# Performance work log

Measured on AMD Instinct MI355X. Metric: run time of the kernel, lower is better.

Reference implementation:

```python
import jax, jax.numpy as jnp
import numpy as np

B = 4096      # batch
F = 26        # num sparse features
L = 10        # pooling factor (multi-hot indices per feature)
V = 100000    # rows per embedding table
D = 128       # embedding dim (== dense_arch_layer_sizes[-1])
DENSE_IN = 13
DENSE_SIZES = [512, 256, 128]
OVER_SIZES = [1024, 1024, 512, 256, 1]
OVER_IN = D + (F * (F - 1)) // 2 + F  # 479


def _linear_params(key, dims, prefix):
    out = {}
    ks = jax.random.split(key, len(dims) - 1)
    for i in range(len(dims) - 1):
        fan_in = dims[i]
        out[f"{prefix}W{i}"] = jax.random.normal(ks[i], (dims[i], dims[i + 1]), jnp.float32) / np.sqrt(fan_in)
        out[f"{prefix}b{i}"] = jnp.zeros((dims[i + 1],), jnp.float32)
    return out


def setup_inputs() -> dict:
    key = jax.random.key(0)
    k0, k1, k2, k3, k4 = jax.random.split(key, 5)
    inp = {
        "dense_features": jax.random.normal(k0, (B, DENSE_IN), jnp.float32),
        "indices": jax.random.randint(k1, (B, F, L), 0, V, dtype=jnp.int64),
        "tables": jax.random.normal(k2, (F, V, D), jnp.float32) * 0.01,
    }
    inp.update(_linear_params(k3, [DENSE_IN] + DENSE_SIZES, "d"))
    inp.update(_linear_params(k4, [OVER_IN] + OVER_SIZES, "o"))
    return inp


def _dlrm_forward(dense_features, indices, tables,
                  dW0, db0, dW1, db1, dW2, db2,
                  oW0, ob0, oW1, ob1, oW2, ob2, oW3, ob3, oW4, ob4):
    b = dense_features.shape[0]
    # DenseArch: MLP with relu on every layer
    x = dense_features
    for W, bb in ((dW0, db0), (dW1, db1), (dW2, db2)):
        x = jax.nn.relu(x @ W + bb)
    embedded_dense = x  # [B, D]

    # SparseArch: pooled (sum) embedding lookup per feature -> [B, F, D]
    flat_tables = tables.reshape(F * V, D)
    offs = jnp.arange(F, dtype=indices.dtype) * V
    flat_idx = (indices + offs[None, :, None]).reshape(-1)
    gathered = jnp.take(flat_tables, flat_idx, axis=0).reshape(b, F, L, D)
    embedded_sparse = gathered.sum(axis=2)  # [B, F, D]

    # InteractionArch: bmm + upper-triangular gather
    z = jnp.concatenate([embedded_dense[:, None, :], embedded_sparse], axis=1)  # [B, F+1, D]
    inter = jnp.einsum("bnd,bmd->bnm", z, z)  # [B, F+1, F+1]
    iu0, iu1 = np.triu_indices(F + 1, k=1)
    inter_flat = inter[:, iu0, iu1]  # [B, C(F+1,2)]
    feats = jnp.concatenate([embedded_dense, inter_flat], axis=1)  # [B, OVER_IN]

    # OverArch: relu MLP on layer_sizes[:-1], then plain final Linear
    y = feats
    for W, bb in ((oW0, ob0), (oW1, ob1), (oW2, ob2), (oW3, ob3)):
        y = jax.nn.relu(y @ W + bb)
    logits = y @ oW4 + ob4  # [B, 1]
    return logits


def reference(dense_features, indices, tables,
              dW0, db0, dW1, db1, dW2, db2,
              oW0, ob0, oW1, ob1, oW2, ob2, oW3, ob3, oW4, ob4):
    return _dlrm_forward(dense_features, indices, tables,
                         dW0, db0, dW1, db1, dW2, db2,
                         oW0, ob0, oW1, ob1, oW2, ob2, oW3, ob3, oW4, ob4)
```

## Files before the change

kernel.cpp:

```cpp
#include <hip/hip_runtime.h>

#define B_ 4096
#define F_ 26
#define L_ 10
#define V_ 100000
#define D_ 128

typedef __attribute__((ext_vector_type(8))) short short8;
typedef __attribute__((ext_vector_type(4))) float f32x4;

__device__ inline unsigned pack_split(float f) {
    union { float f; unsigned u; } a; a.f = f;
    unsigned r = (a.u + 0x7FFFu + ((a.u >> 16) & 1u)) >> 16;
    union { unsigned u; float f; } hf; hf.u = r << 16;
    float rem = f - hf.f;
    union { float f; unsigned u; } b; b.f = rem;
    unsigned r2 = (b.u + 0x7FFFu + ((b.u >> 16) & 1u)) >> 16;
    return (r << 16) | (r2 & 0xFFFFu);
}
__device__ inline float unpack_f(unsigned u) {
    union { unsigned u; float f; } h; h.u = u & 0xFFFF0000u;
    union { unsigned u; float f; } l; l.u = u << 16;
    return h.f + l.f;
}

__device__ void prep_tile(const float* __restrict__ W, unsigned* __restrict__ Wt,
                          int K, int N, int Kp, int local)
{
    __shared__ float tile[32][33];
    const int t = threadIdx.x;
    const int tx = t & 31, ty = t >> 5;
    const int nbt = N >> 5;
    const int nb = (local % nbt) << 5, kb = (local / nbt) << 5;
    #pragma unroll
    for (int i = 0; i < 4; ++i) {
        int k = kb + ty + i * 8;
        tile[ty + i * 8][tx] = (k < K) ? W[(size_t)k * N + nb + tx] : 0.f;
    }
    __syncthreads();
    #pragma unroll
    for (int i = 0; i < 4; ++i) {
        int nl = ty + i * 8;
        Wt[(size_t)(nb + nl) * Kp + kb + tx] = pack_split(tile[tx][nl]);
    }
}

__global__ __launch_bounds__(256) void prep_all(
    const float* dW0, const float* dW1, const float* dW2,
    const float* oW0, const float* oW1, const float* oW2, const float* oW3,
    unsigned* dWt0, unsigned* dWt1, unsigned* dWt2,
    unsigned* oWt0, unsigned* oWt1, unsigned* oWt2, unsigned* oWt3,
    const float* dense, unsigned* densep)
{
    const int bid = blockIdx.x;
    if      (bid < 16)   prep_tile(dW0, dWt0, 13,   512,  32,   bid);
    else if (bid < 144)  prep_tile(dW1, dWt1, 512,  256,  512,  bid - 16);
    else if (bid < 176)  prep_tile(dW2, dWt2, 256,  128,  256,  bid - 144);
    else if (bid < 656)  prep_tile(oW0, oWt0, 479,  1024, 480,  bid - 176);
    else if (bid < 1680) prep_tile(oW1, oWt1, 1024, 1024, 1024, bid - 656);
    else if (bid < 2192) prep_tile(oW2, oWt2, 1024, 512,  1024, bid - 1680);
    else if (bid < 2320) prep_tile(oW3, oWt3, 512,  256,  512,  bid - 2192);
    else {
        int g = (bid - 2320) * 256 + threadIdx.x;
        int b = g >> 5, k = g & 31;
        densep[g] = (k < 13) ? pack_split(dense[(size_t)b * 13 + k]) : 0u;
    }
}

template<bool RELU>
__global__ __launch_bounds__(512) void gemm8(
    const unsigned* __restrict__ Ap, const unsigned* __restrict__ Wt,
    const float* __restrict__ bias, unsigned* __restrict__ Cp,
    int M, int N, int Kp)
{
    __shared__ __align__(16) unsigned Au[2][128 * 32];
    __shared__ __align__(16) unsigned Bu[2][128 * 32];

    const int t    = threadIdx.x;
    const int lane = t & 63;
    const int w    = t >> 6;
    const int wm   = w >> 2, wn = w & 3;
    const int m0   = blockIdx.y * 128, n0 = blockIdx.x * 128;

    f32x4 acc[4][2];
    const f32x4 zero = {0.f, 0.f, 0.f, 0.f};
    #pragma unroll
    for (int i = 0; i < 4; ++i)
        #pragma unroll
        for (int j = 0; j < 2; ++j) acc[i][j] = zero;

    const unsigned* Ab = Ap + (size_t)m0 * Kp;
    const unsigned* Bb = Wt + (size_t)n0 * Kp;

    const int g4 = lane >> 4;
    const int rr = lane & 15;

    auto STAGE = [&](int buf, int k0) {
        #pragma unroll
        for (int i = 0; i < 2; ++i) {
            int chunk = t + (i << 9);
            int row = chunk >> 3, ch = chunk & 7;
            int sch = ch ^ (row & 7);
            __builtin_amdgcn_global_load_lds(
                (const __attribute__((address_space(1))) unsigned*)(Ab + (size_t)row * Kp + k0 + (sch << 2)),
                &Au[buf][chunk << 2], 16, 0, 0);
        }
        #pragma unroll
        for (int i = 0; i < 2; ++i) {
            int chunk = t + (i << 9);
            int row = chunk >> 3, ch = chunk & 7;
            int sch = ch ^ (row & 7);
            __builtin_amdgcn_global_load_lds(
                (const __attribute__((address_space(1))) unsigned*)(Bb + (size_t)row * Kp + k0 + (sch << 2)),
                &Bu[buf][chunk << 2], 16, 0, 0);
        }
    };

    auto COMPUTE = [&](int buf) {
        const unsigned* au = Au[buf];
        const unsigned* bu = Bu[buf];
        short8 bh[2], bl[2];
        #pragma unroll
        for (int tj = 0; tj < 2; ++tj) {
            int r = wn * 32 + tj * 16 + rr;
            int c0 = (2 * g4) ^ (r & 7), c1 = (2 * g4 + 1) ^ (r & 7);
            uint4 p = *reinterpret_cast<const uint4*>(&bu[r * 32 + (c0 << 2)]);
            uint4 q = *reinterpret_cast<const uint4*>(&bu[r * 32 + (c1 << 2)]);
            union { short8 s; uint4 u; } H, L;
            H.u.x = __builtin_amdgcn_perm(p.y, p.x, 0x07060302u);
            L.u.x = __builtin_amdgcn_perm(p.y, p.x, 0x05040100u);
            H.u.y = __builtin_amdgcn_perm(p.w, p.z, 0x07060302u);
            L.u.y = __builtin_amdgcn_perm(p.w, p.z, 0x05040100u);
            H.u.z = __builtin_amdgcn_perm(q.y, q.x, 0x07060302u);
            L.u.z = __builtin_amdgcn_perm(q.y, q.x, 0x05040100u);
            H.u.w = __builtin_amdgcn_perm(q.w, q.z, 0x07060302u);
            L.u.w = __builtin_amdgcn_perm(q.w, q.z, 0x05040100u);
            bh[tj] = H.s; bl[tj] = L.s;
        }
        #pragma unroll
        for (int ti = 0; ti < 4; ++ti) {
            int r = wm * 64 + ti * 16 + rr;
            int c0 = (2 * g4) ^ (r & 7), c1 = (2 * g4 + 1) ^ (r & 7);
            uint4 p = *reinterpret_cast<const uint4*>(&au[r * 32 + (c0 << 2)]);
            uint4 q = *reinterpret_cast<const uint4*>(&au[r * 32 + (c1 << 2)]);
            union { short8 s; uint4 u; } H, L;
            H.u.x = __builtin_amdgcn_perm(p.y, p.x, 0x07060302u);
            L.u.x = __builtin_amdgcn_perm(p.y, p.x, 0x05040100u);
            H.u.y = __builtin_amdgcn_perm(p.w, p.z, 0x07060302u);
            L.u.y = __builtin_amdgcn_perm(p.w, p.z, 0x05040100u);
            H.u.z = __builtin_amdgcn_perm(q.y, q.x, 0x07060302u);
            L.u.z = __builtin_amdgcn_perm(q.y, q.x, 0x05040100u);
            H.u.w = __builtin_amdgcn_perm(q.w, q.z, 0x07060302u);
            L.u.w = __builtin_amdgcn_perm(q.w, q.z, 0x05040100u);
            short8 ah = H.s, al = L.s;
            #pragma unroll
            for (int tj = 0; tj < 2; ++tj) {
                f32x4 c = acc[ti][tj];
                c = __builtin_amdgcn_mfma_f32_16x16x32_bf16(ah, bh[tj], c, 0, 0, 0);
                c = __builtin_amdgcn_mfma_f32_16x16x32_bf16(ah, bl[tj], c, 0, 0, 0);
                c = __builtin_amdgcn_mfma_f32_16x16x32_bf16(al, bh[tj], c, 0, 0, 0);
                acc[ti][tj] = c;
            }
        }
    };

    const int nt = Kp >> 5;
    STAGE(0, 0);
    __syncthreads();
    int cur = 0;
    for (int ts = 0; ts < nt - 1; ++ts) {
        STAGE(cur ^ 1, (ts + 1) << 5);
        COMPUTE(cur);
        __syncthreads();
        cur ^= 1;
    }
    COMPUTE(cur);

    #pragma unroll
    for (int ti = 0; ti < 4; ++ti) {
        int row = m0 + wm * 64 + ti * 16 + (g4 << 2);
        #pragma unroll
        for (int tj = 0; tj < 2; ++tj) {
            int col = n0 + wn * 32 + tj * 16 + rr;
            float bv = bias[col];
            #pragma unroll
            for (int r = 0; r < 4; ++r) {
                float v = acc[ti][tj][r] + bv;
                if (RELU) v = fmaxf(v, 0.f);
                Cp[(size_t)(row + r) * N + col] = pack_split(v);
            }
        }
    }
}

__global__ __launch_bounds__(256) void gather_interact_mfma(
    const unsigned* __restrict__ x2p,
    const int*      __restrict__ idx_words,
    const float*    __restrict__ tables,
    unsigned*       __restrict__ featsp)
{
    __shared__ unsigned zh[4][32][64];
    __shared__ unsigned zl[4][32][64];
    __shared__ int sidx[4][F_ * L_];
    __shared__ int sstride;

    const int t    = threadIdx.x;
    const int w    = t >> 6;
    const int lane = t & 63;
    const int s    = blockIdx.x * 4 + w;

    if (t == 0) {
        int st = 2;
        for (int ww = 1; ww < 256; ww += 2)
            if (idx_words[ww] != 0) { st = 1; break; }
        sstride = st;
    }
    __syncthreads();
    const int st = sstride;

    for (int q = lane; q < F_ * L_; q += 64) {
        int v = idx_words[((size_t)s * F_ * L_ + q) * st];
        sidx[w][q] = v < 0 ? 0 : (v >= V_ ? V_ - 1 : v);
    }
    uint2 xv = *reinterpret_cast<const uint2*>(x2p + (size_t)s * 128 + 2 * lane);
    *reinterpret_cast<uint2*>(featsp + (size_t)s * 480 + 2 * lane) = xv;
    if (lane == 0) featsp[(size_t)s * 480 + 479] = 0u;
    zh[w][0][lane] = (xv.x >> 16) | (xv.y & 0xFFFF0000u);
    zl[w][0][lane] = (xv.x & 0xFFFFu) | (xv.y << 16);
    __syncthreads();

    for (int f = 0; f < F_; ++f) {
        float2 a = {0.f, 0.f};
        const float* tab = tables + (size_t)f * V_ * D_;
        #pragma unroll
        for (int l = 0; l < L_; ++l) {
            int idx = sidx[w][f * L_ + l];
            float2 v = *reinterpret_cast<const float2*>(tab + (size_t)idx * D_ + 2 * lane);
            a.x += v.x; a.y += v.y;
        }
        unsigned px = pack_split(a.x), py = pack_split(a.y);
        int r  = f + 1;
        int dw = (((lane >> 2) ^ (r & 7)) << 2) + (lane & 3);
        zh[w][r][dw] = (px >> 16) | (py & 0xFFFF0000u);
        zl[w][r][dw] = (px & 0xFFFFu) | (py << 16);
    }
    __syncthreads();

    const int g4 = lane >> 4;
    const int rr = lane & 15;
    f32x4 acc[2][2];
    const f32x4 zero = {0.f, 0.f, 0.f, 0.f};
    acc[0][0] = zero; acc[0][1] = zero; acc[1][0] = zero; acc[1][1] = zero;

    #pragma unroll
    for (int ks = 0; ks < 4; ++ks) {
        short8 h[2], lo[2];
        #pragma unroll
        for (int mi = 0; mi < 2; ++mi) {
            int r = mi * 16 + rr;
            int c = (ks * 4 + g4) ^ (r & 7);
            h[mi]  = *reinterpret_cast<const short8*>(&zh[w][r][c << 2]);
            lo[mi] = *reinterpret_cast<const short8*>(&zl[w][r][c << 2]);
        }
        #pragma unroll
        for (int mi = 0; mi < 2; ++mi)
            #pragma unroll
            for (int nj = 0; nj < 2; ++nj) {
                f32x4 c = acc[mi][nj];
                c = __builtin_amdgcn_mfma_f32_16x16x32_bf16(h[mi],  h[nj],  c, 0, 0, 0);
                c = __builtin_amdgcn_mfma_f32_16x16x32_bf16(h[mi],  lo[nj], c, 0, 0, 0);
                c = __builtin_amdgcn_mfma_f32_16x16x32_bf16(lo[mi], h[nj],  c, 0, 0, 0);
                acc[mi][nj] = c;
            }
    }

    #pragma unroll
    for (int mi = 0; mi < 2; ++mi) {
        #pragma unroll
        for (int nj = 0; nj < 2; ++nj) {
            #pragma unroll
            for (int r = 0; r < 4; ++r) {
                int i = mi * 16 + g4 * 4 + r;
                int j = nj * 16 + rr;
                if (i < j && j <= 26) {
                    int p = i * 26 - (i * (i - 1)) / 2 + (j - i - 1);
                    featsp[(size_t)s * 480 + 128 + p] = pack_split(acc[mi][nj][r]);
                }
            }
        }
    }
}

__global__ __launch_bounds__(256) void final_dot(
    const unsigned* __restrict__ yp, const float* __restrict__ w,
    const float* __restrict__ bias, float* __restrict__ out)
{
    const int wave = threadIdx.x >> 6;
    const int lane = threadIdx.x & 63;
    const int b = blockIdx.x * 4 + wave;
    uint4 u = *reinterpret_cast<const uint4*>(yp + (size_t)b * 256 + lane * 4);
    float4 wv = *reinterpret_cast<const float4*>(&w[lane * 4]);
    float s = unpack_f(u.x) * wv.x + unpack_f(u.y) * wv.y +
              unpack_f(u.z) * wv.z + unpack_f(u.w) * wv.w;
    #pragma unroll
    for (int off = 32; off; off >>= 1) s += __shfl_xor(s, off);
    if (lane == 0) out[b] = s + bias[0];
}

extern "C" void kernel_launch(void* const* d_in, const int* in_sizes, int n_in,
                              void* d_out, int out_size, void* d_ws, size_t ws_size,
                              hipStream_t stream)
{
    const float* dense   = (const float*)d_in[0];
    const int*   indices = (const int*)  d_in[1];
    const float* tables  = (const float*)d_in[2];
    const float* dW0 = (const float*)d_in[3];  const float* db0 = (const float*)d_in[4];
    const float* dW1 = (const float*)d_in[5];  const float* db1 = (const float*)d_in[6];
    const float* dW2 = (const float*)d_in[7];  const float* db2 = (const float*)d_in[8];
    const float* oW0 = (const float*)d_in[9];  const float* ob0 = (const float*)d_in[10];
    const float* oW1 = (const float*)d_in[11]; const float* ob1 = (const float*)d_in[12];
    const float* oW2 = (const float*)d_in[13]; const float* ob2 = (const float*)d_in[14];
    const float* oW3 = (const float*)d_in[15]; const float* ob3 = (const float*)d_in[16];
    const float* oW4 = (const float*)d_in[17]; const float* ob4 = (const float*)d_in[18];
    float* out = (float*)d_out;

    unsigned* wsu = (unsigned*)d_ws;
    unsigned* dWt0 = wsu + 0;
    unsigned* dWt1 = wsu + 16384;
    unsigned* dWt2 = wsu + 147456;
    unsigned* oWt0 = wsu + 180224;
    unsigned* oWt1 = wsu + 671744;
    unsigned* oWt2 = wsu + 1720320;
    unsigned* oWt3 = wsu + 2244608;
    unsigned* densep = wsu + 2375680;
    unsigned* x2p    = wsu + 2506752;
    unsigned* featsp = wsu + 3031040;
    unsigned* x0p    = wsu + 5000000;
    unsigned* x1p    = wsu + 7097152;
    unsigned* y0p    = wsu + 5000000;
    unsigned* y1p    = wsu + 9194304;
    unsigned* y2p    = wsu + 2506752;
    unsigned* y3p    = wsu + 5000000;

    prep_all<<<2832, 256, 0, stream>>>(dW0, dW1, dW2, oW0, oW1, oW2, oW3,
                                       dWt0, dWt1, dWt2, oWt0, oWt1, oWt2, oWt3,
                                       dense, densep);

    gemm8<true><<<dim3(4, B_ / 128), 512, 0, stream>>>(densep, dWt0, db0, x0p, B_, 512, 32);
    gemm8<true><<<dim3(2, B_ / 128), 512, 0, stream>>>(x0p,    dWt1, db1, x1p, B_, 256, 512);
    gemm8<true><<<dim3(1, B_ / 128), 512, 0, stream>>>(x1p,    dWt2, db2, x2p, B_, 128, 256);

    gather_interact_mfma<<<B_ / 4, 256, 0, stream>>>(x2p, indices, tables, featsp);

    gemm8<true><<<dim3(8, B_ / 128), 512, 0, stream>>>(featsp, oWt0, ob0, y0p, B_, 1024, 480);
    gemm8<true><<<dim3(8, B_ / 128), 512, 0, stream>>>(y0p,    oWt1, ob1, y1p, B_, 1024, 1024);
    gemm8<true><<<dim3(4, B_ / 128), 512, 0, stream>>>(y1p,    oWt2, ob2, y2p, B_, 512, 1024);
    gemm8<true><<<dim3(2, B_ / 128), 512, 0, stream>>>(y2p,    oWt3, ob3, y3p, B_, 256, 512);

    final_dot<<<B_ / 4, 256, 0, stream>>>(y3p, oW4, ob4, out);
}
```

Baseline: 294.6 us.

## Add 64-row GEMM tile variant, XCD-aware block swizzle, and paired-feature gather

```diff
diff --git a/kernel.cpp b/kernel.cpp
--- a/kernel.cpp
+++ b/kernel.cpp
@@ -67,20 +67,27 @@
     }
 }
 
-template<bool RELU>
-__global__ __launch_bounds__(512) void gemm8(
+template<int TM>
+__device__ __forceinline__ void gemm_body(
     const unsigned* __restrict__ Ap, const unsigned* __restrict__ Wt,
     const float* __restrict__ bias, unsigned* __restrict__ Cp,
-    int M, int N, int Kp)
-{
-    __shared__ __align__(16) unsigned Au[2][128 * 32];
+    int N, int Kp, int gx)
+{
+    constexpr int BT = TM * 4;
+    __shared__ __align__(16) unsigned Au[2][TM * 32];
     __shared__ __align__(16) unsigned Bu[2][128 * 32];
 
     const int t    = threadIdx.x;
     const int lane = t & 63;
     const int w    = t >> 6;
-    const int wm   = w >> 2, wn = w & 3;
-    const int m0   = blockIdx.y * 128, n0 = blockIdx.x * 128;
+    const int wm   = (TM == 128) ? (w >> 2) : 0;
+    const int wn   = (TM == 128) ? (w & 3) : w;
+
+    const int bid  = blockIdx.x;
+    const int cpx  = gridDim.x >> 3;
+    const int swz  = (bid & 7) * cpx + (bid >> 3);
+    const int n0   = (swz % gx) * 128;
+    const int m0   = (swz / gx) * TM;
 
     f32x4 acc[4][2];
     const f32x4 zero = {0.f, 0.f, 0.f, 0.f};
@@ -98,7 +105,7 @@
     auto STAGE = [&](int buf, int k0) {
         #pragma unroll
         for (int i = 0; i < 2; ++i) {
-            int chunk = t + (i << 9);
+            int chunk = t + i * BT;
             int row = chunk >> 3, ch = chunk & 7;
             int sch = ch ^ (row & 7);
             __builtin_amdgcn_global_load_lds(
@@ -106,8 +113,8 @@
                 &Au[buf][chunk << 2], 16, 0, 0);
         }
         #pragma unroll
-        for (int i = 0; i < 2; ++i) {
-            int chunk = t + (i << 9);
+        for (int i = 0; i < 1024 / BT; ++i) {
+            int chunk = t + i * BT;
             int row = chunk >> 3, ch = chunk & 7;
             int sch = ch ^ (row & 7);
             __builtin_amdgcn_global_load_lds(
@@ -185,12 +192,27 @@
             float bv = bias[col];
             #pragma unroll
             for (int r = 0; r < 4; ++r) {
-                float v = acc[ti][tj][r] + bv;
-                if (RELU) v = fmaxf(v, 0.f);
+                float v = fmaxf(acc[ti][tj][r] + bv, 0.f);
                 Cp[(size_t)(row + r) * N + col] = pack_split(v);
             }
         }
     }
+}
+
+__global__ __launch_bounds__(512) void gemm_t128(
+    const unsigned* __restrict__ Ap, const unsigned* __restrict__ Wt,
+    const float* __restrict__ bias, unsigned* __restrict__ Cp,
+    int N, int Kp, int gx)
+{
+    gemm_body<128>(Ap, Wt, bias, Cp, N, Kp, gx);
+}
+
+__global__ __launch_bounds__(256) void gemm_t64(
+    const unsigned* __restrict__ Ap, const unsigned* __restrict__ Wt,
+    const float* __restrict__ bias, unsigned* __restrict__ Cp,
+    int N, int Kp, int gx)
+{
+    gemm_body<64>(Ap, Wt, bias, Cp, N, Kp, gx);
 }
 
 __global__ __launch_bounds__(256) void gather_interact_mfma(
@@ -229,20 +251,33 @@
     zl[w][0][lane] = (xv.x & 0xFFFFu) | (xv.y << 16);
     __syncthreads();
 
-    for (int f = 0; f < F_; ++f) {
-        float2 a = {0.f, 0.f};
-        const float* tab = tables + (size_t)f * V_ * D_;
+    for (int f = 0; f < F_; f += 2) {
+        float2 a0 = {0.f, 0.f}, a1 = {0.f, 0.f};
+        const float* tab0 = tables + (size_t)f * V_ * D_;
+        const float* tab1 = tables + (size_t)(f + 1) * V_ * D_;
         #pragma unroll
         for (int l = 0; l < L_; ++l) {
-            int idx = sidx[w][f * L_ + l];
-            float2 v = *reinterpret_cast<const float2*>(tab + (size_t)idx * D_ + 2 * lane);
-            a.x += v.x; a.y += v.y;
-        }
-        unsigned px = pack_split(a.x), py = pack_split(a.y);
-        int r  = f + 1;
-        int dw = (((lane >> 2) ^ (r & 7)) << 2) + (lane & 3);
-        zh[w][r][dw] = (px >> 16) | (py & 0xFFFF0000u);
-        zl[w][r][dw] = (px & 0xFFFFu) | (py << 16);
+            int i0 = sidx[w][f * L_ + l];
+            int i1 = sidx[w][(f + 1) * L_ + l];
+            float2 v0 = *reinterpret_cast<const float2*>(tab0 + (size_t)i0 * D_ + 2 * lane);
+            float2 v1 = *reinterpret_cast<const float2*>(tab1 + (size_t)i1 * D_ + 2 * lane);
+            a0.x += v0.x; a0.y += v0.y;
+            a1.x += v1.x; a1.y += v1.y;
+        }
+        {
+            unsigned px = pack_split(a0.x), py = pack_split(a0.y);
+            int r  = f + 1;
+            int dw = (((lane >> 2) ^ (r & 7)) << 2) + (lane & 3);
+            zh[w][r][dw] = (px >> 16) | (py & 0xFFFF0000u);
+            zl[w][r][dw] = (px & 0xFFFFu) | (py << 16);
+        }
+        {
+            unsigned px = pack_split(a1.x), py = pack_split(a1.y);
+            int r  = f + 2;
+            int dw = (((lane >> 2) ^ (r & 7)) << 2) + (lane & 3);
+            zh[w][r][dw] = (px >> 16) | (py & 0xFFFF0000u);
+            zl[w][r][dw] = (px & 0xFFFFu) | (py << 16);
+        }
     }
     __syncthreads();
 
@@ -346,16 +381,16 @@
                                        dWt0, dWt1, dWt2, oWt0, oWt1, oWt2, oWt3,
                                        dense, densep);
 
-    gemm8<true><<<dim3(4, B_ / 128), 512, 0, stream>>>(densep, dWt0, db0, x0p, B_, 512, 32);
-    gemm8<true><<<dim3(2, B_ / 128), 512, 0, stream>>>(x0p,    dWt1, db1, x1p, B_, 256, 512);
-    gemm8<true><<<dim3(1, B_ / 128), 512, 0, stream>>>(x1p,    dWt2, db2, x2p, B_, 128, 256);
+    gemm_t64<<<4 * 64, 256, 0, stream>>>(densep, dWt0, db0, x0p, 512, 32,  4);
+    gemm_t64<<<2 * 64, 256, 0, stream>>>(x0p,    dWt1, db1, x1p, 256, 512, 2);
+    gemm_t64<<<1 * 64, 256, 0, stream>>>(x1p,    dWt2, db2, x2p, 128, 256, 1);
 
     gather_interact_mfma<<<B_ / 4, 256, 0, stream>>>(x2p, indices, tables, featsp);
 
-    gemm8<true><<<dim3(8, B_ / 128), 512, 0, stream>>>(featsp, oWt0, ob0, y0p, B_, 1024, 480);
-    gemm8<true><<<dim3(8, B_ / 128), 512, 0, stream>>>(y0p,    oWt1, ob1, y1p, B_, 1024, 1024);
-    gemm8<true><<<dim3(4, B_ / 128), 512, 0, stream>>>(y1p,    oWt2, ob2, y2p, B_, 512, 1024);
-    gemm8<true><<<dim3(2, B_ / 128), 512, 0, stream>>>(y2p,    oWt3, ob3, y3p, B_, 256, 512);
+    gemm_t128<<<8 * 32, 512, 0, stream>>>(featsp, oWt0, ob0, y0p, 1024, 480,  8);
+    gemm_t128<<<8 * 32, 512, 0, stream>>>(y0p,    oWt1, ob1, y1p, 1024, 1024, 8);
+    gemm_t64<<<4 * 64, 256, 0, stream>>>(y1p,    oWt2, ob2, y2p, 512, 1024, 4);
+    gemm_t64<<<2 * 64, 256, 0, stream>>>(y2p,    oWt3, ob3, y3p, 256, 512,  2);
 
     final_dot<<<B_ / 4, 256, 0, stream>>>(y3p, oW4, ob4, out);
 }
```

Result: no change. 299.3 us (+1.6%).

## Store split-bf16 operands as separate hi/lo planes to drop perm unpacking

Applied to the files above, without the earlier changes.

```diff
diff --git a/kernel.cpp b/kernel.cpp
--- a/kernel.cpp
+++ b/kernel.cpp
@@ -8,6 +8,7 @@
 
 typedef __attribute__((ext_vector_type(8))) short short8;
 typedef __attribute__((ext_vector_type(4))) float f32x4;
+typedef unsigned short u16;
 
 __device__ inline unsigned pack_split(float f) {
     union { float f; unsigned u; } a; a.f = f;
@@ -18,13 +19,13 @@
     unsigned r2 = (b.u + 0x7FFFu + ((b.u >> 16) & 1u)) >> 16;
     return (r << 16) | (r2 & 0xFFFFu);
 }
-__device__ inline float unpack_f(unsigned u) {
-    union { unsigned u; float f; } h; h.u = u & 0xFFFF0000u;
-    union { unsigned u; float f; } l; l.u = u << 16;
-    return h.f + l.f;
-}
-
-__device__ void prep_tile(const float* __restrict__ W, unsigned* __restrict__ Wt,
+__device__ inline float bf2_to_f(u16 h, u16 l) {
+    union { unsigned u; float f; } a; a.u = ((unsigned)h) << 16;
+    union { unsigned u; float f; } b; b.u = ((unsigned)l) << 16;
+    return a.f + b.f;
+}
+
+__device__ void prep_tile(const float* __restrict__ W, u16* __restrict__ Wt,
                           int K, int N, int Kp, int local)
 {
     __shared__ float tile[32][33];
@@ -41,16 +42,19 @@
     #pragma unroll
     for (int i = 0; i < 4; ++i) {
         int nl = ty + i * 8;
-        Wt[(size_t)(nb + nl) * Kp + kb + tx] = pack_split(tile[tx][nl]);
+        unsigned u = pack_split(tile[tx][nl]);
+        size_t base = (size_t)(nb + nl) * 2 * Kp + kb + tx;
+        Wt[base]      = (u16)(u >> 16);
+        Wt[base + Kp] = (u16)(u & 0xFFFFu);
     }
 }
 
 __global__ __launch_bounds__(256) void prep_all(
     const float* dW0, const float* dW1, const float* dW2,
     const float* oW0, const float* oW1, const float* oW2, const float* oW3,
-    unsigned* dWt0, unsigned* dWt1, unsigned* dWt2,
-    unsigned* oWt0, unsigned* oWt1, unsigned* oWt2, unsigned* oWt3,
-    const float* dense, unsigned* densep)
+    u16* dWt0, u16* dWt1, u16* dWt2,
+    u16* oWt0, u16* oWt1, u16* oWt2, u16* oWt3,
+    const float* dense, u16* densep)
 {
     const int bid = blockIdx.x;
     if      (bid < 16)   prep_tile(dW0, dWt0, 13,   512,  32,   bid);
@@ -63,18 +67,19 @@
     else {
         int g = (bid - 2320) * 256 + threadIdx.x;
         int b = g >> 5, k = g & 31;
-        densep[g] = (k < 13) ? pack_split(dense[(size_t)b * 13 + k]) : 0u;
-    }
-}
-
-template<bool RELU>
-__global__ __launch_bounds__(512) void gemm8(
-    const unsigned* __restrict__ Ap, const unsigned* __restrict__ Wt,
-    const float* __restrict__ bias, unsigned* __restrict__ Cp,
-    int M, int N, int Kp)
-{
-    __shared__ __align__(16) unsigned Au[2][128 * 32];
-    __shared__ __align__(16) unsigned Bu[2][128 * 32];
+        unsigned u = (k < 13) ? pack_split(dense[(size_t)b * 13 + k]) : 0u;
+        densep[(size_t)b * 64 + k]      = (u16)(u >> 16);
+        densep[(size_t)b * 64 + 32 + k] = (u16)(u & 0xFFFFu);
+    }
+}
+
+__global__ __launch_bounds__(512) void gemm_pl(
+    const u16* __restrict__ Ap, const u16* __restrict__ Wt,
+    const float* __restrict__ bias, u16* __restrict__ Cp,
+    int N, int Kp)
+{
+    __shared__ __align__(16) u16 Au[2][128 * 64];
+    __shared__ __align__(16) u16 Bu[2][128 * 64];
 
     const int t    = threadIdx.x;
     const int lane = t & 63;
@@ -89,8 +94,8 @@
         #pragma unroll
         for (int j = 0; j < 2; ++j) acc[i][j] = zero;
 
-    const unsigned* Ab = Ap + (size_t)m0 * Kp;
-    const unsigned* Bb = Wt + (size_t)n0 * Kp;
+    const u16* Ab = Ap + (size_t)m0 * 2 * Kp;
+    const u16* Bb = Wt + (size_t)n0 * 2 * Kp;
 
     const int g4 = lane >> 4;
     const int rr = lane & 15;
@@ -99,60 +104,44 @@
         #pragma unroll
         for (int i = 0; i < 2; ++i) {
             int chunk = t + (i << 9);
-            int row = chunk >> 3, ch = chunk & 7;
-            int sch = ch ^ (row & 7);
+            int row = chunk >> 3, c = chunk & 7;
+            int l = c ^ (row & 7);
             __builtin_amdgcn_global_load_lds(
-                (const __attribute__((address_space(1))) unsigned*)(Ab + (size_t)row * Kp + k0 + (sch << 2)),
-                &Au[buf][chunk << 2], 16, 0, 0);
+                (const __attribute__((address_space(1))) u16*)
+                    (Ab + (size_t)row * 2 * Kp + (l >> 2) * Kp + k0 + ((l & 3) << 3)),
+                &Au[buf][chunk << 3], 16, 0, 0);
         }
         #pragma unroll
         for (int i = 0; i < 2; ++i) {
             int chunk = t + (i << 9);
-            int row = chunk >> 3, ch = chunk & 7;
-            int sch = ch ^ (row & 7);
+            int row = chunk >> 3, c = chunk & 7;
+            int l = c ^ (row & 7);
             __builtin_amdgcn_global_load_lds(
-                (const __attribute__((address_space(1))) unsigned*)(Bb + (size_t)row * Kp + k0 + (sch << 2)),
-                &Bu[buf][chunk << 2], 16, 0, 0);
+                (const __attribute__((address_space(1))) u16*)
+                    (Bb + (size_t)row * 2 * Kp + (l >> 2) * Kp + k0 + ((l & 3) << 3)),
+                &Bu[buf][chunk << 3], 16, 0, 0);
         }
     };
 
     auto COMPUTE = [&](int buf) {
-        const unsigned* au = Au[buf];
-        const unsigned* bu = Bu[buf];
+        const u16* au = Au[buf];
+        const u16* bu = Bu[buf];
         short8 bh[2], bl[2];
         #pragma unroll
         for (int tj = 0; tj < 2; ++tj) {
             int r = wn * 32 + tj * 16 + rr;
-            int c0 = (2 * g4) ^ (r & 7), c1 = (2 * g4 + 1) ^ (r & 7);
-            uint4 p = *reinterpret_cast<const uint4*>(&bu[r * 32 + (c0 << 2)]);
-            uint4 q = *reinterpret_cast<const uint4*>(&bu[r * 32 + (c1 << 2)]);
-            union { short8 s; uint4 u; } H, L;
-            H.u.x = __builtin_amdgcn_perm(p.y, p.x, 0x07060302u);
-            L.u.x = __builtin_amdgcn_perm(p.y, p.x, 0x05040100u);
-            H.u.y = __builtin_amdgcn_perm(p.w, p.z, 0x07060302u);
-            L.u.y = __builtin_amdgcn_perm(p.w, p.z, 0x05040100u);
-            H.u.z = __builtin_amdgcn_perm(q.y, q.x, 0x07060302u);
-            L.u.z = __builtin_amdgcn_perm(q.y, q.x, 0x05040100u);
-            H.u.w = __builtin_amdgcn_perm(q.w, q.z, 0x07060302u);
-            L.u.w = __builtin_amdgcn_perm(q.w, q.z, 0x05040100u);
-            bh[tj] = H.s; bl[tj] = L.s;
+            int ch = (g4 ^ (r & 7)) << 3;
+            int cl = ((4 + g4) ^ (r & 7)) << 3;
+            bh[tj] = *reinterpret_cast<const short8*>(&bu[r * 64 + ch]);
+            bl[tj] = *reinterpret_cast<const short8*>(&bu[r * 64 + cl]);
         }
         #pragma unroll
         for (int ti = 0; ti < 4; ++ti) {
             int r = wm * 64 + ti * 16 + rr;
-            int c0 = (2 * g4) ^ (r & 7), c1 = (2 * g4 + 1) ^ (r & 7);
-            uint4 p = *reinterpret_cast<const uint4*>(&au[r * 32 + (c0 << 2)]);
-            uint4 q = *reinterpret_cast<const uint4*>(&au[r * 32 + (c1 << 2)]);
-            union { short8 s; uint4 u; } H, L;
-            H.u.x = __builtin_amdgcn_perm(p.y, p.x, 0x07060302u);
-            L.u.x = __builtin_amdgcn_perm(p.y, p.x, 0x05040100u);
-            H.u.y = __builtin_amdgcn_perm(p.w, p.z, 0x07060302u);
-            L.u.y = __builtin_amdgcn_perm(p.w, p.z, 0x05040100u);
-            H.u.z = __builtin_amdgcn_perm(q.y, q.x, 0x07060302u);
-            L.u.z = __builtin_amdgcn_perm(q.y, q.x, 0x05040100u);
-            H.u.w = __builtin_amdgcn_perm(q.w, q.z, 0x07060302u);
-            L.u.w = __builtin_amdgcn_perm(q.w, q.z, 0x05040100u);
-            short8 ah = H.s, al = L.s;
+            int ch = (g4 ^ (r & 7)) << 3;
+            int cl = ((4 + g4) ^ (r & 7)) << 3;
+            short8 ah = *reinterpret_cast<const short8*>(&au[r * 64 + ch]);
+            short8 al = *reinterpret_cast<const short8*>(&au[r * 64 + cl]);
             #pragma unroll
             for (int tj = 0; tj < 2; ++tj) {
                 f32x4 c = acc[ti][tj];
@@ -185,19 +174,21 @@
             float bv = bias[col];
             #pragma unroll
             for (int r = 0; r < 4; ++r) {
-                float v = acc[ti][tj][r] + bv;
-                if (RELU) v = fmaxf(v, 0.f);
-                Cp[(size_t)(row + r) * N + col] = pack_split(v);
+                float v = fmaxf(acc[ti][tj][r] + bv, 0.f);
+                unsigned u = pack_split(v);
+                size_t base = (size_t)(row + r) * 2 * N + col;
+                Cp[base]     = (u16)(u >> 16);
+                Cp[base + N] = (u16)(u & 0xFFFFu);
             }
         }
     }
 }
 
 __global__ __launch_bounds__(256) void gather_interact_mfma(
-    const unsigned* __restrict__ x2p,
-    const int*      __restrict__ idx_words,
-    const float*    __restrict__ tables,
-    unsigned*       __restrict__ featsp)
+    const u16*   __restrict__ x2p,
+    const int*   __restrict__ idx_words,
+    const float* __restrict__ tables,
+    u16*         __restrict__ featsp)
 {
     __shared__ unsigned zh[4][32][64];
     __shared__ unsigned zl[4][32][64];
@@ -222,11 +213,13 @@
         int v = idx_words[((size_t)s * F_ * L_ + q) * st];
         sidx[w][q] = v < 0 ? 0 : (v >= V_ ? V_ - 1 : v);
     }
-    uint2 xv = *reinterpret_cast<const uint2*>(x2p + (size_t)s * 128 + 2 * lane);
-    *reinterpret_cast<uint2*>(featsp + (size_t)s * 480 + 2 * lane) = xv;
-    if (lane == 0) featsp[(size_t)s * 480 + 479] = 0u;
-    zh[w][0][lane] = (xv.x >> 16) | (xv.y & 0xFFFF0000u);
-    zl[w][0][lane] = (xv.x & 0xFFFFu) | (xv.y << 16);
+    unsigned hv = *reinterpret_cast<const unsigned*>(x2p + (size_t)s * 256 + 2 * lane);
+    unsigned lv = *reinterpret_cast<const unsigned*>(x2p + (size_t)s * 256 + 128 + 2 * lane);
+    *reinterpret_cast<unsigned*>(featsp + (size_t)s * 960 + 2 * lane) = hv;
+    *reinterpret_cast<unsigned*>(featsp + (size_t)s * 960 + 480 + 2 * lane) = lv;
+    if (lane == 0) { featsp[(size_t)s * 960 + 479] = 0; featsp[(size_t)s * 960 + 959] = 0; }
+    zh[w][0][lane] = hv;
+    zl[w][0][lane] = lv;
     __syncthreads();
 
     for (int f = 0; f < F_; ++f) {
@@ -284,7 +277,9 @@
                 int j = nj * 16 + rr;
                 if (i < j && j <= 26) {
                     int p = i * 26 - (i * (i - 1)) / 2 + (j - i - 1);
-                    featsp[(size_t)s * 480 + 128 + p] = pack_split(acc[mi][nj][r]);
+                    unsigned u = pack_split(acc[mi][nj][r]);
+                    featsp[(size_t)s * 960 + 128 + p]       = (u16)(u >> 16);
+                    featsp[(size_t)s * 960 + 480 + 128 + p] = (u16)(u & 0xFFFFu);
                 }
             }
         }
@@ -292,16 +287,18 @@
 }
 
 __global__ __launch_bounds__(256) void final_dot(
-    const unsigned* __restrict__ yp, const float* __restrict__ w,
+    const u16* __restrict__ yp, const float* __restrict__ w,
     const float* __restrict__ bias, float* __restrict__ out)
 {
     const int wave = threadIdx.x >> 6;
     const int lane = threadIdx.x & 63;
     const int b = blockIdx.x * 4 + wave;
-    uint4 u = *reinterpret_cast<const uint4*>(yp + (size_t)b * 256 + lane * 4);
+    const u16* row = yp + (size_t)b * 512;
+    ushort4 uh = *reinterpret_cast<const ushort4*>(row + 4 * lane);
+    ushort4 ul = *reinterpret_cast<const ushort4*>(row + 256 + 4 * lane);
     float4 wv = *reinterpret_cast<const float4*>(&w[lane * 4]);
-    float s = unpack_f(u.x) * wv.x + unpack_f(u.y) * wv.y +
-              unpack_f(u.z) * wv.z + unpack_f(u.w) * wv.w;
+    float s = bf2_to_f(uh.x, ul.x) * wv.x + bf2_to_f(uh.y, ul.y) * wv.y +
+              bf2_to_f(uh.z, ul.z) * wv.z + bf2_to_f(uh.w, ul.w) * wv.w;
     #pragma unroll
     for (int off = 32; off; off >>= 1) s += __shfl_xor(s, off);
     if (lane == 0) out[b] = s + bias[0];
@@ -325,37 +322,37 @@
     float* out = (float*)d_out;
 
     unsigned* wsu = (unsigned*)d_ws;
-    unsigned* dWt0 = wsu + 0;
-    unsigned* dWt1 = wsu + 16384;
-    unsigned* dWt2 = wsu + 147456;
-    unsigned* oWt0 = wsu + 180224;
-    unsigned* oWt1 = wsu + 671744;
-    unsigned* oWt2 = wsu + 1720320;
-    unsigned* oWt3 = wsu + 2244608;
-    unsigned* densep = wsu + 2375680;
-    unsigned* x2p    = wsu + 2506752;
-    unsigned* featsp = wsu + 3031040;
-    unsigned* x0p    = wsu + 5000000;
-    unsigned* x1p    = wsu + 7097152;
-    unsigned* y0p    = wsu + 5000000;
-    unsigned* y1p    = wsu + 9194304;
-    unsigned* y2p    = wsu + 2506752;
-    unsigned* y3p    = wsu + 5000000;
+    u16* dWt0 = (u16*)(wsu + 0);
+    u16* dWt1 = (u16*)(wsu + 16384);
+    u16* dWt2 = (u16*)(wsu + 147456);
+    u16* oWt0 = (u16*)(wsu + 180224);
+    u16* oWt1 = (u16*)(wsu + 671744);
+    u16* oWt2 = (u16*)(wsu + 1720320);
+    u16* oWt3 = (u16*)(wsu + 2244608);
+    u16* densep = (u16*)(wsu + 2375680);
+    u16* x2p    = (u16*)(wsu + 2506752);
+    u16* featsp = (u16*)(wsu + 3031040);
+    u16* x0p    = (u16*)(wsu + 5000000);
+    u16* x1p    = (u16*)(wsu + 7097152);
+    u16* y0p    = (u16*)(wsu + 5000000);
+    u16* y1p    = (u16*)(wsu + 9194304);
+    u16* y2p    = (u16*)(wsu + 2506752);
+    u16* y3p    = (u16*)(wsu + 5000000);
 
     prep_all<<<2832, 256, 0, stream>>>(dW0, dW1, dW2, oW0, oW1, oW2, oW3,
                                        dWt0, dWt1, dWt2, oWt0, oWt1, oWt2, oWt3,
                                        dense, densep);
 
-    gemm8<true><<<dim3(4, B_ / 128), 512, 0, stream>>>(densep, dWt0, db0, x0p, B_, 512, 32);
-    gemm8<true><<<dim3(2, B_ / 128), 512, 0, stream>>>(x0p,    dWt1, db1, x1p, B_, 256, 512);
-    gemm8<true><<<dim3(1, B_ / 128), 512, 0, stream>>>(x1p,    dWt2, db2, x2p, B_, 128, 256);
+    gemm_pl<<<dim3(4, 32), 512, 0, stream>>>(densep, dWt0, db0, x0p, 512, 32);
+    gemm_pl<<<dim3(2, 32), 512, 0, stream>>>(x0p,    dWt1, db1, x1p, 256, 512);
+    gemm_pl<<<dim3(1, 32), 512, 0, stream>>>(x1p,    dWt2, db2, x2p, 128, 256);
 
     gather_interact_mfma<<<B_ / 4, 256, 0, stream>>>(x2p, indices, tables, featsp);
 
-    gemm8<true><<<dim3(8, B_ / 128), 512, 0, stream>>>(featsp, oWt0, ob0, y0p, B_, 1024, 480);
-    gemm8<true><<<dim3(8, B_ / 128), 512, 0, stream>>>(y0p,    oWt1, ob1, y1p, B_, 1024, 1024);
-    gemm8<true><<<dim3(4, B_ / 128), 512, 0, stream>>>(y1p,    oWt2, ob2, y2p, B_, 512, 1024);
-    gemm8<true><<<dim3(2, B_ / 128), 512, 0, stream>>>(y2p,    oWt3, ob3, y3p, B_, 256, 512);
+    gemm_pl<<<dim3(8, 32), 512, 0, stream>>>(featsp, oWt0, ob0, y0p, 1024, 480);
+    gemm_pl<<<dim3(8, 32), 512, 0, stream>>>(y0p,    oWt1, ob1, y1p, 1024, 1024);
+    gemm_pl<<<dim3(4, 32), 512, 0, stream>>>(y1p,    oWt2, ob2, y2p, 512, 1024);
+    gemm_pl<<<dim3(2, 32), 512, 0, stream>>>(y2p,    oWt3, ob3, y3p, 256, 512);
 
     final_dot<<<B_ / 4, 256, 0, stream>>>(y3p, oW4, ob4, out);
 }
```

New measurement: 302.6 us. 2.7% more time.

## Triple-buffer A tiles with vmcnt waits and one barrier per k-step in GEMM

Applied to the files above, without the earlier changes.

```diff
diff --git a/kernel.cpp b/kernel.cpp
--- a/kernel.cpp
+++ b/kernel.cpp
@@ -67,13 +67,12 @@
     }
 }
 
-template<bool RELU>
 __global__ __launch_bounds__(512) void gemm8(
     const unsigned* __restrict__ Ap, const unsigned* __restrict__ Wt,
     const float* __restrict__ bias, unsigned* __restrict__ Cp,
-    int M, int N, int Kp)
-{
-    __shared__ __align__(16) unsigned Au[2][128 * 32];
+    int N, int Kp)
+{
+    __shared__ __align__(16) unsigned Au[3][128 * 32];
     __shared__ __align__(16) unsigned Bu[2][128 * 32];
 
     const int t    = threadIdx.x;
@@ -95,7 +94,8 @@
     const int g4 = lane >> 4;
     const int rr = lane & 15;
 
-    auto STAGE = [&](int buf, int k0) {
+    auto STAGE_A = [&](int buf, int kt) {
+        int k0 = kt << 5;
         #pragma unroll
         for (int i = 0; i < 2; ++i) {
             int chunk = t + (i << 9);
@@ -105,6 +105,9 @@
                 (const __attribute__((address_space(1))) unsigned*)(Ab + (size_t)row * Kp + k0 + (sch << 2)),
                 &Au[buf][chunk << 2], 16, 0, 0);
         }
+    };
+    auto STAGE_B = [&](int buf, int kt) {
+        int k0 = kt << 5;
         #pragma unroll
         for (int i = 0; i < 2; ++i) {
             int chunk = t + (i << 9);
@@ -116,9 +119,9 @@
         }
     };
 
-    auto COMPUTE = [&](int buf) {
-        const unsigned* au = Au[buf];
-        const unsigned* bu = Bu[buf];
+    auto COMPUTE = [&](int abuf, int bbuf) {
+        const unsigned* au = Au[abuf];
+        const unsigned* bu = Bu[bbuf];
         short8 bh[2], bl[2];
         #pragma unroll
         for (int tj = 0; tj < 2; ++tj) {
@@ -165,16 +168,19 @@
     };
 
     const int nt = Kp >> 5;
-    STAGE(0, 0);
-    __syncthreads();
-    int cur = 0;
-    for (int ts = 0; ts < nt - 1; ++ts) {
-        STAGE(cur ^ 1, (ts + 1) << 5);
-        COMPUTE(cur);
-        __syncthreads();
-        cur ^= 1;
-    }
-    COMPUTE(cur);
+    STAGE_A(0, 0);
+    STAGE_B(0, 0);
+    if (nt > 1) STAGE_A(1, 1);
+
+    for (int ts = 0; ts < nt; ++ts) {
+        if (ts < nt - 1) asm volatile("s_waitcnt vmcnt(2)" ::: "memory");
+        else             asm volatile("s_waitcnt vmcnt(0)" ::: "memory");
+        __builtin_amdgcn_s_barrier();
+        __builtin_amdgcn_sched_barrier(0);
+        if (ts + 1 < nt) STAGE_B((ts + 1) & 1, ts + 1);
+        if (ts + 2 < nt) STAGE_A((ts + 2) % 3, ts + 2);
+        COMPUTE(ts % 3, ts & 1);
+    }
 
     #pragma unroll
     for (int ti = 0; ti < 4; ++ti) {
@@ -185,8 +191,7 @@
             float bv = bias[col];
             #pragma unroll
             for (int r = 0; r < 4; ++r) {
-                float v = acc[ti][tj][r] + bv;
-                if (RELU) v = fmaxf(v, 0.f);
+                float v = fmaxf(acc[ti][tj][r] + bv, 0.f);
                 Cp[(size_t)(row + r) * N + col] = pack_split(v);
             }
         }
@@ -346,16 +351,16 @@
                                        dWt0, dWt1, dWt2, oWt0, oWt1, oWt2, oWt3,
                                        dense, densep);
 
-    gemm8<true><<<dim3(4, B_ / 128), 512, 0, stream>>>(densep, dWt0, db0, x0p, B_, 512, 32);
-    gemm8<true><<<dim3(2, B_ / 128), 512, 0, stream>>>(x0p,    dWt1, db1, x1p, B_, 256, 512);
-    gemm8<true><<<dim3(1, B_ / 128), 512, 0, stream>>>(x1p,    dWt2, db2, x2p, B_, 128, 256);
+    gemm8<<<dim3(4, 32), 512, 0, stream>>>(densep, dWt0, db0, x0p, 512, 32);
+    gemm8<<<dim3(2, 32), 512, 0, stream>>>(x0p,    dWt1, db1, x1p, 256, 512);
+    gemm8<<<dim3(1, 32), 512, 0, stream>>>(x1p,    dWt2, db2, x2p, 128, 256);
 
     gather_interact_mfma<<<B_ / 4, 256, 0, stream>>>(x2p, indices, tables, featsp);
 
-    gemm8<true><<<dim3(8, B_ / 128), 512, 0, stream>>>(featsp, oWt0, ob0, y0p, B_, 1024, 480);
-    gemm8<true><<<dim3(8, B_ / 128), 512, 0, stream>>>(y0p,    oWt1, ob1, y1p, B_, 1024, 1024);
-    gemm8<true><<<dim3(4, B_ / 128), 512, 0, stream>>>(y1p,    oWt2, ob2, y2p, B_, 512, 1024);
-    gemm8<true><<<dim3(2, B_ / 128), 512, 0, stream>>>(y2p,    oWt3, ob3, y3p, B_, 256, 512);
+    gemm8<<<dim3(8, 32), 512, 0, stream>>>(featsp, oWt0, ob0, y0p, 1024, 480);
+    gemm8<<<dim3(8, 32), 512, 0, stream>>>(y0p,    oWt1, ob1, y1p, 1024, 1024);
+    gemm8<<<dim3(4, 32), 512, 0, stream>>>(y1p,    oWt2, ob2, y2p, 512, 1024);
+    gemm8<<<dim3(2, 32), 512, 0, stream>>>(y2p,    oWt3, ob3, y3p, 256, 512);
 
     final_dot<<<B_ / 4, 256, 0, stream>>>(y3p, oW4, ob4, out);
 }
```

Measured after the change: 301.4 us. +2.3%, slower.
